# Optimization experiments

Measured on AMD Instinct MI355X. Metric: run time of the kernel, lower is better.

## Reference

```python
import jax, jax.numpy as jnp
import numpy as np

N = 65536          # total atoms
M = 12             # max neighbors
ORIG = 92          # orig_atom_fea_len
NBR = 41           # nbr_fea_len
AF = 64            # atom_fea_len
NCONV = 3
HF = 128           # h_fea_len
N0 = 1024          # number of crystals
EPS = 1e-5


def _glorot(key, shape):
    fan_in, fan_out = shape[0], shape[-1]
    lim = np.sqrt(6.0 / (fan_in + fan_out)).astype(np.float32)
    return jax.random.uniform(key, shape, jnp.float32, -lim, lim)


def setup_inputs() -> dict:
    key = jax.random.key(0)
    ks = jax.random.split(key, 16)
    atom_fea = jax.random.normal(ks[0], (N, ORIG), jnp.float32)
    nbr_fea = jax.random.normal(ks[1], (N, M, NBR), jnp.float32)
    nbr_fea_idx = jax.random.randint(ks[2], (N, M), 0, N, jnp.int32)
    # flat segment ids: ~64 atoms per crystal, contiguous (mimics ragged idx lists)
    crystal_idx = jnp.repeat(jnp.arange(N0, dtype=jnp.int32), N // N0)
    # parameters
    emb_w = _glorot(ks[3], (ORIG, AF)); emb_b = jnp.zeros((AF,), jnp.float32)
    conv_fc_w = _glorot(ks[4], (NCONV, 2 * AF + NBR, 2 * AF))
    conv_fc_b = jnp.zeros((NCONV, 2 * AF), jnp.float32)
    conv_bn1_g = jnp.ones((NCONV, 2 * AF), jnp.float32)
    conv_bn1_b = jnp.zeros((NCONV, 2 * AF), jnp.float32)
    conv_bn2_g = jnp.ones((NCONV, AF), jnp.float32)
    conv_bn2_b = jnp.zeros((NCONV, AF), jnp.float32)
    fc1_w = _glorot(ks[5], (AF, HF)); fc1_b = jnp.zeros((HF,), jnp.float32)
    out1_w = _glorot(ks[6], (HF, HF // 2)); out1_b = jnp.zeros((HF // 2,), jnp.float32)
    out2_w = _glorot(ks[7], (HF // 2, 1)); out2_b = jnp.zeros((1,), jnp.float32)
    return dict(atom_fea=atom_fea, nbr_fea=nbr_fea, nbr_fea_idx=nbr_fea_idx,
                crystal_idx=crystal_idx, emb_w=emb_w, emb_b=emb_b,
                conv_fc_w=conv_fc_w, conv_fc_b=conv_fc_b,
                conv_bn1_g=conv_bn1_g, conv_bn1_b=conv_bn1_b,
                conv_bn2_g=conv_bn2_g, conv_bn2_b=conv_bn2_b,
                fc1_w=fc1_w, fc1_b=fc1_b, out1_w=out1_w, out1_b=out1_b,
                out2_w=out2_w, out2_b=out2_b)


def _batchnorm(x, g, b):
    # training-mode BatchNorm1d over axis 0, biased variance, eps=1e-5
    mu = jnp.mean(x, axis=0)
    var = jnp.var(x, axis=0)
    return (x - mu) * jax.lax.rsqrt(var + EPS) * g + b


def _conv_layer(afea, nbr_fea, nbr_idx, w, b, g1, b1, g2, b2):
    # gather neighbor atom features: (N, M, AF)
    atom_nbr = afea[nbr_idx]
    self_fea = jnp.broadcast_to(afea[:, None, :], (N, M, AF))
    total = jnp.concatenate([self_fea, atom_nbr, nbr_fea], axis=-1)  # (N, M, 2AF+NBR)
    gated = jnp.einsum('nmf,fg->nmg', total, w) + b                  # (N, M, 2AF)
    gated = _batchnorm(gated.reshape(-1, 2 * AF), g1, b1).reshape(N, M, 2 * AF)
    filt, core = jnp.split(gated, 2, axis=-1)
    nbr_sumed = jnp.sum(jax.nn.sigmoid(filt) * jax.nn.softplus(core), axis=1)  # scatter-sum over nbrs
    nbr_sumed = _batchnorm(nbr_sumed, g2, b2)
    return jax.nn.softplus(afea + nbr_sumed)


def reference(atom_fea, nbr_fea, nbr_fea_idx, crystal_idx, emb_w, emb_b,
              conv_fc_w, conv_fc_b, conv_bn1_g, conv_bn1_b, conv_bn2_g, conv_bn2_b,
              fc1_w, fc1_b, out1_w, out1_b, out2_w, out2_b):
    afea = atom_fea @ emb_w + emb_b                 # (N, AF)
    identity = afea
    for i in range(NCONV):
        afea = _conv_layer(afea, nbr_fea, nbr_fea_idx,
                           conv_fc_w[i], conv_fc_b[i],
                           conv_bn1_g[i], conv_bn1_b[i],
                           conv_bn2_g[i], conv_bn2_b[i])
        afea = afea + identity
        identity = afea
    # ragged per-crystal mean pooling via segment_sum
    sums = jax.ops.segment_sum(afea, crystal_idx, num_segments=N0)
    counts = jax.ops.segment_sum(jnp.ones((N,), afea.dtype), crystal_idx, num_segments=N0)
    crys = sums / jnp.maximum(counts, 1.0)[:, None]  # (N0, AF)
    crys = jax.nn.softplus(crys) @ fc1_w + fc1_b
    crys = jax.nn.softplus(crys)                     # (N0, HF) == repr
    out = jax.nn.softplus(crys @ out1_w + out1_b) @ out2_w + out2_b  # (N0, 1)
    return out, crys
```

## Files before the change

### kernel.cpp

```cpp
#include <hip/hip_runtime.h>

#define NATOM 65536
#define MNBR 12
#define NMROW (NATOM*MNBR)
#define ORIG 92
#define NBRF 41
#define AF 64
#define HF 128
#define NCRYS 1024
#define EPSBN 1e-5f
#define NBP 48
#define CGRID 2048
#define NTASK 16384

typedef __attribute__((ext_vector_type(8))) short short8;
typedef __attribute__((ext_vector_type(4))) float floatx4;

__device__ __forceinline__ float softplusf_(float x){
    return fmaxf(x,0.f) + __logf(1.f + __expf(-fabsf(x)));
}
__device__ __forceinline__ float sigmoidf_(float x){
    return __builtin_amdgcn_rcpf(1.f + __expf(-x));
}
__device__ __forceinline__ short f2bf(float x){
    unsigned u = __float_as_uint(x);
    u += 0x7fffu + ((u >> 16) & 1u);
    return (short)(u >> 16);
}

__global__ void k_embed(const float* __restrict__ atom_fea, const float* __restrict__ emb_w,
                        const float* __restrict__ emb_b, float* __restrict__ afea,
                        short* __restrict__ abf)
{
    __shared__ float wl[ORIG*AF];
    __shared__ float bl[AF];
    __shared__ float rows[4*ORIG];
    int tid = threadIdx.x;
    for (int i = tid; i < ORIG*AF; i += 256) wl[i] = emb_w[i];
    if (tid < AF) bl[tid] = emb_b[tid];
    __syncthreads();
    for (int t = blockIdx.x; t < NATOM/4; t += gridDim.x) {
        for (int i = tid; i < 4*ORIG; i += 256) rows[i] = atom_fea[t*4*ORIG + i];
        __syncthreads();
        int r = tid >> 6, c = tid & 63;
        float acc = bl[c];
        const float* rp = &rows[r*ORIG];
        #pragma unroll 4
        for (int k = 0; k < ORIG; ++k) acc += rp[k] * wl[k*AF + c];
        int n = t*4 + r;
        afea[n*AF + c] = acc;
        abf[n*AF + c] = f2bf(acc);
        __syncthreads();
    }
}

__global__ void k_prep_nbr(const float* __restrict__ nbr_fea, short* __restrict__ nbf)
{
    int g = blockIdx.x*256 + threadIdx.x;
    int row = g / NBP, k = g % NBP;
    float v = (k < NBRF) ? nbr_fea[row*NBRF + k] : 0.f;
    nbf[g] = f2bf(v);
}

__global__ void k_prep_w(const float* __restrict__ W, short* __restrict__ wt2)
{
    int g = blockIdx.x*256 + threadIdx.x;
    int j = g & 7, c = (g >> 3) & 127, q = (g >> 10) & 3, ks = g >> 12;
    int k = ks*32 + q*8 + j;
    wt2[g] = (k < 169) ? f2bf(W[k*128 + c]) : (short)0;
}

template<int PASS2>
__global__ __launch_bounds__(256, 3)
void k_conv(const short* __restrict__ abf, const short* __restrict__ nbf,
            const int* __restrict__ nbr_idx, const short* __restrict__ wt2,
            const float* __restrict__ bias,
            float* __restrict__ stats1, const float* __restrict__ bn1ss,
            float* __restrict__ nsum, float* __restrict__ stats2)
{
    __shared__ __align__(16) short stg[2][6432];
    __shared__ float pbuf[4*12*17];

    int tid = threadIdx.x;
    int lane = tid & 63, wave = tid >> 6;
    int l15 = lane & 15, q = lane >> 4;
    int cf = wave*16 + l15;
    int cc = 64 + cf;

    short8 wf[6][2];
    #pragma unroll
    for (int ks = 0; ks < 6; ++ks) {
        wf[ks][0] = *(const short8*)(wt2 + ((ks*4+q)*128 + cf)*8);
        wf[ks][1] = *(const short8*)(wt2 + ((ks*4+q)*128 + cc)*8);
    }
    float bs0 = bias[cf], bs1 = bias[cc];
    float sc0=0.f, sh0=0.f, sc1=0.f, sh1=0.f;
    if (PASS2) { sc0=bn1ss[cf]; sh0=bn1ss[128+cf]; sc1=bn1ss[cc]; sh1=bn1ss[128+cc]; }

    int kind[3], ldso[3], nrow[3]; long gco[3];
    #pragma unroll
    for (int s = 0; s < 3; ++s) {
        int i = tid + s*256;
        if (i < 384)      { kind[s]=0; int row=i>>3, c=i&7; nrow[s]=row; ldso[s]=row*72+c*8; gco[s]=c*8; }
        else if (i < 672) { kind[s]=1; int j=i-384; int row=j/6, c=j%6; nrow[s]=0; ldso[s]=3456+row*56+c*8; gco[s]=row*48+c*8; }
        else if (i < 704) { kind[s]=2; int j=i-672; int a=j>>3, c=j&7; nrow[s]=0; ldso[s]=6144+a*72+c*8; gco[s]=a*64+c*8; }
        else              { kind[s]=3; nrow[s]=0; ldso[s]=0; gco[s]=0; }
    }
    int art[3], nvo[3], evo[3], svo[3];
    #pragma unroll
    for (int rt = 0; rt < 3; ++rt) {
        int r = rt*16 + l15;
        art[rt] = r/12;
        nvo[rt] = r*72 + q*8;
        evo[rt] = 3456 + r*56 + q*8;
        svo[rt] = 6144 + art[rt]*72 + q*8;
    }

    float s_acc[2]={0.f,0.f}, s2_acc[2]={0.f,0.f};
    float st2s = 0.f, st2q = 0.f;
    const short8 zf = {0,0,0,0,0,0,0,0};
    float* pb = pbuf + wave*(12*17);
    const int bt = blockIdx.x;

    int nid[3];
    short8 hold[3];
    #pragma unroll
    for (int s = 0; s < 3; ++s)
        if (kind[s]==0) nid[s] = nbr_idx[bt*48 + nrow[s]];
    #pragma unroll
    for (int s = 0; s < 3; ++s) {
        if (kind[s]==0)      hold[s] = *(const short8*)(abf + (unsigned)nid[s]*64u + gco[s]);
        else if (kind[s]==1) hold[s] = *(const short8*)(nbf + (long)bt*2304 + gco[s]);
        else if (kind[s]==2) hold[s] = *(const short8*)(abf + (unsigned)bt*256u + gco[s]);
    }
    #pragma unroll
    for (int s = 0; s < 3; ++s)
        if (kind[s]==0) nid[s] = nbr_idx[(bt+CGRID)*48 + nrow[s]];
    #pragma unroll
    for (int s = 0; s < 3; ++s)
        if (kind[s] < 3) *(short8*)(&stg[0][0] + ldso[s]) = hold[s];
    __syncthreads();

    #pragma unroll 2
    for (int k = 0; k < 8; ++k) {
        int b = bt + k*CGRID;
        if (k < 7) {
            int bn = b + CGRID;
            #pragma unroll
            for (int s = 0; s < 3; ++s) {
                if (kind[s]==0)      hold[s] = *(const short8*)(abf + (unsigned)nid[s]*64u + gco[s]);
                else if (kind[s]==1) hold[s] = *(const short8*)(nbf + (long)bn*2304 + gco[s]);
                else if (kind[s]==2) hold[s] = *(const short8*)(abf + (unsigned)bn*256u + gco[s]);
            }
            if (k < 6) {
                #pragma unroll
                for (int s = 0; s < 3; ++s)
                    if (kind[s]==0) nid[s] = nbr_idx[(bn+CGRID)*48 + nrow[s]];
            }
        }

        const short* sb = &stg[k & 1][0];
        floatx4 acc[3][2];
        #pragma unroll
        for (int rt=0; rt<3; ++rt) {
            acc[rt][0] = (floatx4){bs0,bs0,bs0,bs0};
            acc[rt][1] = (floatx4){bs1,bs1,bs1,bs1};
        }
        #pragma unroll
        for (int rt = 0; rt < 3; ++rt) {
            short8 sv0 = *(const short8*)(sb + svo[rt]);
            short8 sv1 = *(const short8*)(sb + svo[rt] + 32);
            short8 nv0 = *(const short8*)(sb + nvo[rt]);
            short8 nv1 = *(const short8*)(sb + nvo[rt] + 32);
            short8 ev0 = *(const short8*)(sb + evo[rt]);
            short8 ev1 = (q < 2) ? *(const short8*)(sb + evo[rt] + 32) : zf;
            #pragma unroll
            for (int ct = 0; ct < 2; ++ct) {
                acc[rt][ct] = __builtin_amdgcn_mfma_f32_16x16x32_bf16(sv0, wf[0][ct], acc[rt][ct], 0,0,0);
                acc[rt][ct] = __builtin_amdgcn_mfma_f32_16x16x32_bf16(sv1, wf[1][ct], acc[rt][ct], 0,0,0);
                acc[rt][ct] = __builtin_amdgcn_mfma_f32_16x16x32_bf16(nv0, wf[2][ct], acc[rt][ct], 0,0,0);
                acc[rt][ct] = __builtin_amdgcn_mfma_f32_16x16x32_bf16(nv1, wf[3][ct], acc[rt][ct], 0,0,0);
                acc[rt][ct] = __builtin_amdgcn_mfma_f32_16x16x32_bf16(ev0, wf[4][ct], acc[rt][ct], 0,0,0);
                acc[rt][ct] = __builtin_amdgcn_mfma_f32_16x16x32_bf16(ev1, wf[5][ct], acc[rt][ct], 0,0,0);
            }
        }

        if (!PASS2) {
            #pragma unroll
            for (int ct=0; ct<2; ++ct)
                #pragma unroll
                for (int rt=0; rt<3; ++rt)
                    #pragma unroll
                    for (int r=0; r<4; ++r) {
                        float v = acc[rt][ct][r];
                        s_acc[ct] += v; s2_acc[ct] += v*v;
                    }
        } else {
            #pragma unroll
            for (int rt=0; rt<3; ++rt) {
                float part = 0.f;
                #pragma unroll
                for (int r=0; r<4; ++r) {
                    float f = acc[rt][0][r]*sc0 + sh0;
                    float g = acc[rt][1][r]*sc1 + sh1;
                    part += sigmoidf_(f) * softplusf_(g);
                }
                pb[(rt*4+q)*17 + l15] = part;
            }
            int a = lane >> 4, c16 = lane & 15;
            float s = pb[(3*a+0)*17 + c16] + pb[(3*a+1)*17 + c16] + pb[(3*a+2)*17 + c16];
            nsum[(b*4 + a)*AF + wave*16 + c16] = s;
            st2s += s; st2q += s*s;
        }

        if (k < 7) {
            short* db = &stg[(k + 1) & 1][0];
            #pragma unroll
            for (int s = 0; s < 3; ++s)
                if (kind[s] < 3) *(short8*)(db + ldso[s]) = hold[s];
        }
        __syncthreads();
    }

    if (!PASS2) {
        #pragma unroll
        for (int ct=0; ct<2; ++ct) {
            float s = s_acc[ct], s2 = s2_acc[ct];
            s  += __shfl_xor(s, 16);  s  += __shfl_xor(s, 32);
            s2 += __shfl_xor(s2, 16); s2 += __shfl_xor(s2, 32);
            if (q == 0) {
                int c = ct ? cc : cf;
                atomicAdd(&stats1[c], s);
                atomicAdd(&stats1[128 + c], s2);
            }
        }
    } else {
        st2s += __shfl_xor(st2s, 16); st2s += __shfl_xor(st2s, 32);
        st2q += __shfl_xor(st2q, 16); st2q += __shfl_xor(st2q, 32);
        if (q == 0) {
            atomicAdd(&stats2[cf], st2s);
            atomicAdd(&stats2[64 + cf], st2q);
        }
    }
}

__global__ void k_bn1fin(const float* __restrict__ stats1, const float* __restrict__ g,
                         const float* __restrict__ b, float* __restrict__ bn1ss)
{
    int c = threadIdx.x;
    float mean = stats1[c] * (1.f/NMROW);
    float var  = stats1[128+c] * (1.f/NMROW) - mean*mean;
    float scale = g[c] * rsqrtf(var + EPSBN);
    bn1ss[c] = scale;
    bn1ss[128+c] = b[c] - mean*scale;
}

__global__ void k_update(float* __restrict__ afea, short* __restrict__ abf,
                         const float* __restrict__ nsum,
                         const float* __restrict__ stats2,
                         const float* __restrict__ g2, const float* __restrict__ b2)
{
    int g = blockIdx.x*256 + threadIdx.x;
    int c = g & 63;
    float mean = stats2[c] * (1.f/NATOM);
    float var  = stats2[64+c] * (1.f/NATOM) - mean*mean;
    float scale = g2[c]*rsqrtf(var + EPSBN);
    float shift = b2[c] - mean*scale;
    float ns = nsum[g]*scale + shift;
    float a = afea[g];
    float v = softplusf_(a + ns) + a;
    afea[g] = v; abf[g] = f2bf(v);
}

__global__ void k_pool(const float* __restrict__ afea, const int* __restrict__ cidx,
                       float* __restrict__ pool, float* __restrict__ cnt)
{
    int g = blockIdx.x*256 + threadIdx.x;
    int c = g & 63; int chunk = g >> 6;
    float run = 0.f, rc = 0.f; int cur = -1;
    for (int i = 0; i < 16; ++i) {
        int a = chunk*16 + i;
        int cr = cidx[a];
        float v = afea[a*64 + c];
        if (cr != cur) {
            if (cur >= 0) { atomicAdd(&pool[cur*64+c], run); if (c==0) atomicAdd(&cnt[cur], rc); }
            run = 0.f; rc = 0.f; cur = cr;
        }
        run += v; rc += 1.f;
    }
    atomicAdd(&pool[cur*64+c], run); if (c==0) atomicAdd(&cnt[cur], rc);
}

__global__ void k_head(const float* __restrict__ pool, const float* __restrict__ cnt,
                       const float* __restrict__ fc1w, const float* __restrict__ fc1b,
                       const float* __restrict__ o1w, const float* __restrict__ o1b,
                       const float* __restrict__ o2w, const float* __restrict__ o2b,
                       float* __restrict__ dout)
{
    __shared__ float spv[64], crys[128], h1[64];
    int b = blockIdx.x, tid = threadIdx.x;
    if (tid < 64) {
        float ct = fmaxf(cnt[b], 1.f);
        spv[tid] = softplusf_(pool[b*64+tid] / ct);
    }
    __syncthreads();
    float a = fc1b[tid];
    for (int k = 0; k < 64; ++k) a += spv[k] * fc1w[k*128 + tid];
    float v = softplusf_(a);
    crys[tid] = v;
    dout[NCRYS + b*128 + tid] = v;
    __syncthreads();
    if (tid < 64) {
        float a2 = o1b[tid];
        for (int k = 0; k < 128; ++k) a2 += crys[k] * o1w[k*64 + tid];
        h1[tid] = softplusf_(a2) * o2w[tid];
    }
    __syncthreads();
    if (tid == 0) {
        float s = o2b[0];
        for (int j = 0; j < 64; ++j) s += h1[j];
        dout[b] = s;
    }
}

extern "C" void kernel_launch(void* const* d_in, const int* in_sizes, int n_in,
                              void* d_out, int out_size, void* d_ws, size_t ws_size,
                              hipStream_t stream)
{
    const float* atom_fea = (const float*)d_in[0];
    const float* nbr_fea  = (const float*)d_in[1];
    const int*   nbr_idx  = (const int*)d_in[2];
    const int*   cidx     = (const int*)d_in[3];
    const float* emb_w    = (const float*)d_in[4];
    const float* emb_b    = (const float*)d_in[5];
    const float* cfw      = (const float*)d_in[6];
    const float* cfb      = (const float*)d_in[7];
    const float* bn1g     = (const float*)d_in[8];
    const float* bn1b     = (const float*)d_in[9];
    const float* bn2g     = (const float*)d_in[10];
    const float* bn2b     = (const float*)d_in[11];
    const float* fc1w     = (const float*)d_in[12];
    const float* fc1b     = (const float*)d_in[13];
    const float* o1w      = (const float*)d_in[14];
    const float* o1b      = (const float*)d_in[15];
    const float* o2w      = (const float*)d_in[16];
    const float* o2b      = (const float*)d_in[17];

    float* ws    = (float*)d_ws;
    float* afea  = ws;
    float* nsum  = ws + 4194304;
    short* abf   = (short*)(ws + 8388608);
    short* nbf   = (short*)(ws + 10485760);
    short* wt2   = (short*)(ws + 29360128);
    float* stats = ws + 29372416;
    float* pool  = ws + 29374336;
    float* cnt   = ws + 29439872;

    hipMemsetAsync(stats, 0, (1920 + 65536 + 1024)*sizeof(float), stream);

    k_prep_nbr<<<(NMROW*NBP)/256, 256, 0, stream>>>(nbr_fea, nbf);
    k_embed<<<2048, 256, 0, stream>>>(atom_fea, emb_w, emb_b, afea, abf);

    for (int L = 0; L < 3; ++L) {
        float* st1 = stats + L*640;
        float* ss  = st1 + 256;
        float* st2 = st1 + 512;
        k_prep_w<<<96, 256, 0, stream>>>(cfw + L*169*128, wt2);
        k_conv<0><<<CGRID, 256, 0, stream>>>(abf, nbf, nbr_idx, wt2, cfb + L*128, st1, nullptr, nullptr, nullptr);
        k_bn1fin<<<1, 128, 0, stream>>>(st1, bn1g + L*128, bn1b + L*128, ss);
        k_conv<1><<<CGRID, 256, 0, stream>>>(abf, nbf, nbr_idx, wt2, cfb + L*128, nullptr, ss, nsum, st2);
        k_update<<<16384, 256, 0, stream>>>(afea, abf, nsum, st2, bn2g + L*64, bn2b + L*64);
    }
    k_pool<<<1024, 256, 0, stream>>>(afea, cidx, pool, cnt);
    k_head<<<NCRYS, 128, 0, stream>>>(pool, cnt, fc1w, fc1b, o1w, o1b, o2w, o2b, (float*)d_out);
}
```

Before: 849.7 us.

## Store conv gate pre-activations in bf16 instead of recomputing the conv GEMM

The first conv pass now writes the filter and core pre-activations as packed bf16 pairs to a large workspace buffer. A new lightweight gate kernel then applies BN1, sigmoid and softplus and sums over neighbors, replacing the second full gather-plus-MFMA pass. This trades a recomputed GEMM and gather for about 200 MB of extra write and read traffic per layer, and it rounds the pre-activations to bf16 before BN. The neighbor-feature prep kernel is also vectorised to write 8 bf16 values per thread. The old two-pass path is kept as a fallback when the workspace is too small.

```diff
diff --git a/kernel.cpp b/kernel.cpp
--- a/kernel.cpp
+++ b/kernel.cpp
@@ -27,6 +27,9 @@
     u += 0x7fffu + ((u >> 16) & 1u);
     return (short)(u >> 16);
 }
+__device__ __forceinline__ unsigned packbf(float f, float g){
+    return (unsigned)(unsigned short)f2bf(f) | ((unsigned)(unsigned short)f2bf(g) << 16);
+}
 
 __global__ void k_embed(const float* __restrict__ atom_fea, const float* __restrict__ emb_w,
                         const float* __restrict__ emb_b, float* __restrict__ afea,
@@ -57,9 +60,16 @@
 __global__ void k_prep_nbr(const float* __restrict__ nbr_fea, short* __restrict__ nbf)
 {
     int g = blockIdx.x*256 + threadIdx.x;
-    int row = g / NBP, k = g % NBP;
-    float v = (k < NBRF) ? nbr_fea[row*NBRF + k] : 0.f;
-    nbf[g] = f2bf(v);
+    int row = g / 6, c = g % 6;
+    const float* src = nbr_fea + (long)row*NBRF + c*8;
+    short8 v = {0,0,0,0,0,0,0,0};
+    if (c < 5) {
+        #pragma unroll
+        for (int j = 0; j < 8; ++j) v[j] = f2bf(src[j]);
+    } else {
+        v[0] = f2bf(src[0]);
+    }
+    *(short8*)(nbf + (long)g*8) = v;
 }
 
 __global__ void k_prep_w(const float* __restrict__ W, short* __restrict__ wt2)
@@ -70,16 +80,17 @@
     wt2[g] = (k < 169) ? f2bf(W[k*128 + c]) : (short)0;
 }
 
-template<int PASS2>
+template<int MODE>
 __global__ __launch_bounds__(256, 3)
 void k_conv(const short* __restrict__ abf, const short* __restrict__ nbf,
             const int* __restrict__ nbr_idx, const short* __restrict__ wt2,
             const float* __restrict__ bias,
             float* __restrict__ stats1, const float* __restrict__ bn1ss,
-            float* __restrict__ nsum, float* __restrict__ stats2)
+            float* __restrict__ nsum, float* __restrict__ stats2,
+            unsigned* __restrict__ gpair)
 {
     __shared__ __align__(16) short stg[2][6432];
-    __shared__ float pbuf[4*12*17];
+    __shared__ float pbuf[(MODE==1) ? 4*12*17 : 4];
 
     int tid = threadIdx.x;
     int lane = tid & 63, wave = tid >> 6;
@@ -95,7 +106,7 @@
     }
     float bs0 = bias[cf], bs1 = bias[cc];
     float sc0=0.f, sh0=0.f, sc1=0.f, sh1=0.f;
-    if (PASS2) { sc0=bn1ss[cf]; sh0=bn1ss[128+cf]; sc1=bn1ss[cc]; sh1=bn1ss[128+cc]; }
+    if (MODE==1) { sc0=bn1ss[cf]; sh0=bn1ss[128+cf]; sc1=bn1ss[cc]; sh1=bn1ss[128+cc]; }
 
     int kind[3], ldso[3], nrow[3]; long gco[3];
     #pragma unroll
@@ -119,7 +130,7 @@
     float s_acc[2]={0.f,0.f}, s2_acc[2]={0.f,0.f};
     float st2s = 0.f, st2q = 0.f;
     const short8 zf = {0,0,0,0,0,0,0,0};
-    float* pb = pbuf + wave*(12*17);
+    float* pb = pbuf + ((MODE==1) ? wave*(12*17) : 0);
     const int bt = blockIdx.x;
 
     int nid[3];
@@ -185,7 +196,7 @@
             }
         }
 
-        if (!PASS2) {
+        if (MODE != 1) {
             #pragma unroll
             for (int ct=0; ct<2; ++ct)
                 #pragma unroll
@@ -195,7 +206,17 @@
                         float v = acc[rt][ct][r];
                         s_acc[ct] += v; s2_acc[ct] += v*v;
                     }
-        } else {
+        }
+        if (MODE == 2) {
+            #pragma unroll
+            for (int rt=0; rt<3; ++rt) {
+                unsigned base = (unsigned)(b*48 + rt*16 + q*4)*64u + (unsigned)(wave*16 + l15);
+                #pragma unroll
+                for (int r=0; r<4; ++r)
+                    gpair[base + (unsigned)r*64u] = packbf(acc[rt][0][r], acc[rt][1][r]);
+            }
+        }
+        if (MODE == 1) {
             #pragma unroll
             for (int rt=0; rt<3; ++rt) {
                 float part = 0.f;
@@ -222,7 +243,7 @@
         __syncthreads();
     }
 
-    if (!PASS2) {
+    if (MODE != 1) {
         #pragma unroll
         for (int ct=0; ct<2; ++ct) {
             float s = s_acc[ct], s2 = s2_acc[ct];
@@ -241,6 +262,46 @@
             atomicAdd(&stats2[cf], st2s);
             atomicAdd(&stats2[64 + cf], st2q);
         }
+    }
+}
+
+__global__ __launch_bounds__(256, 4)
+void k_gate(const unsigned* __restrict__ gpair, const float* __restrict__ bn1ss,
+            float* __restrict__ nsum, float* __restrict__ stats2)
+{
+    __shared__ float red[2][4][64];
+    int tid = threadIdx.x;
+    int lane = tid & 63, wave = tid >> 6;
+    float scf = bn1ss[lane],    shf = bn1ss[128+lane];
+    float scc = bn1ss[64+lane], shc = bn1ss[192+lane];
+    float st2s = 0.f, st2q = 0.f;
+    int a0 = blockIdx.x*64 + wave;
+    for (int j = 0; j < 16; ++j) {
+        int atom = a0 + j*4;
+        const unsigned* gp = gpair + (unsigned)atom*12u*64u + lane;
+        unsigned u[12];
+        #pragma unroll
+        for (int i = 0; i < 12; ++i) u[i] = gp[i*64];
+        float s = 0.f;
+        #pragma unroll
+        for (int i = 0; i < 12; ++i) {
+            float f = __uint_as_float(u[i] << 16);
+            float g = __uint_as_float(u[i] & 0xffff0000u);
+            f = f*scf + shf;
+            g = g*scc + shc;
+            s += sigmoidf_(f) * softplusf_(g);
+        }
+        nsum[atom*AF + lane] = s;
+        st2s += s; st2q += s*s;
+    }
+    red[0][wave][lane] = st2s;
+    red[1][wave][lane] = st2q;
+    __syncthreads();
+    if (tid < 64) {
+        float s  = red[0][0][tid] + red[0][1][tid] + red[0][2][tid] + red[0][3][tid];
+        float s2 = red[1][0][tid] + red[1][1][tid] + red[1][2][tid] + red[1][3][tid];
+        atomicAdd(&stats2[tid], s);
+        atomicAdd(&stats2[64 + tid], s2);
     }
 }
 
@@ -355,10 +416,13 @@
     float* stats = ws + 29372416;
     float* pool  = ws + 29374336;
     float* cnt   = ws + 29439872;
+    unsigned* gpair = (unsigned*)(ws + 29440896);
+
+    bool big = ws_size >= (size_t)(29440896 + 50331648) * 4;
 
     hipMemsetAsync(stats, 0, (1920 + 65536 + 1024)*sizeof(float), stream);
 
-    k_prep_nbr<<<(NMROW*NBP)/256, 256, 0, stream>>>(nbr_fea, nbf);
+    k_prep_nbr<<<(NMROW*6)/256, 256, 0, stream>>>(nbr_fea, nbf);
     k_embed<<<2048, 256, 0, stream>>>(atom_fea, emb_w, emb_b, afea, abf);
 
     for (int L = 0; L < 3; ++L) {
@@ -366,9 +430,18 @@
         float* ss  = st1 + 256;
         float* st2 = st1 + 512;
         k_prep_w<<<96, 256, 0, stream>>>(cfw + L*169*128, wt2);
-        k_conv<0><<<CGRID, 256, 0, stream>>>(abf, nbf, nbr_idx, wt2, cfb + L*128, st1, nullptr, nullptr, nullptr);
-        k_bn1fin<<<1, 128, 0, stream>>>(st1, bn1g + L*128, bn1b + L*128, ss);
-        k_conv<1><<<CGRID, 256, 0, stream>>>(abf, nbf, nbr_idx, wt2, cfb + L*128, nullptr, ss, nsum, st2);
+        if (big) {
+            k_conv<2><<<CGRID, 256, 0, stream>>>(abf, nbf, nbr_idx, wt2, cfb + L*128,
+                                                 st1, nullptr, nullptr, nullptr, gpair);
+            k_bn1fin<<<1, 128, 0, stream>>>(st1, bn1g + L*128, bn1b + L*128, ss);
+            k_gate<<<NATOM/64, 256, 0, stream>>>(gpair, ss, nsum, st2);
+        } else {
+            k_conv<0><<<CGRID, 256, 0, stream>>>(abf, nbf, nbr_idx, wt2, cfb + L*128,
+                                                 st1, nullptr, nullptr, nullptr, nullptr);
+            k_bn1fin<<<1, 128, 0, stream>>>(st1, bn1g + L*128, bn1b + L*128, ss);
+            k_conv<1><<<CGRID, 256, 0, stream>>>(abf, nbf, nbr_idx, wt2, cfb + L*128,
+                                                 nullptr, ss, nsum, st2, nullptr);
+        }
         k_update<<<16384, 256, 0, stream>>>(afea, abf, nsum, st2, bn2g + L*64, bn2b + L*64);
     }
     k_pool<<<1024, 256, 0, stream>>>(afea, cidx, pool, cnt);
```

Result: faster. 821.6 us (-3.3%).

## Split conv output channels across 8 waves and vectorize prep/update kernels

Applied to the files above, without the earlier changes.

The conv kernel moves from 256 to 512 threads per block. Each wave now computes one 16-channel column tile (filter or core half) instead of two, which halves its MFMA accumulator and weight registers. In pass 2 the filter waves write sigmoid values to shared memory and the core waves combine them after an extra barrier. The nbr prep and update kernels are vectorized to 8-wide and 4-wide stores, and the edge-feature loads become nontemporal. This aims to raise occupancy and latency hiding, at the cost of an extra __syncthreads and a shared-memory exchange per tile.

```diff
diff --git a/kernel.cpp b/kernel.cpp
--- a/kernel.cpp
+++ b/kernel.cpp
@@ -14,6 +14,7 @@
 #define NTASK 16384
 
 typedef __attribute__((ext_vector_type(8))) short short8;
+typedef __attribute__((ext_vector_type(4))) short shortx4;
 typedef __attribute__((ext_vector_type(4))) float floatx4;
 
 __device__ __forceinline__ float softplusf_(float x){
@@ -57,9 +58,16 @@
 __global__ void k_prep_nbr(const float* __restrict__ nbr_fea, short* __restrict__ nbf)
 {
     int g = blockIdx.x*256 + threadIdx.x;
-    int row = g / NBP, k = g % NBP;
-    float v = (k < NBRF) ? nbr_fea[row*NBRF + k] : 0.f;
-    nbf[g] = f2bf(v);
+    int row = g / 6, c = g % 6;
+    const float* src = nbr_fea + (long)row*NBRF + c*8;
+    short8 v = {0,0,0,0,0,0,0,0};
+    if (c < 5) {
+        #pragma unroll
+        for (int j = 0; j < 8; ++j) v[j] = f2bf(src[j]);
+    } else {
+        v[0] = f2bf(src[0]);
+    }
+    *(short8*)(nbf + (long)g*8) = v;
 }
 
 __global__ void k_prep_w(const float* __restrict__ W, short* __restrict__ wt2)
@@ -71,7 +79,7 @@
 }
 
 template<int PASS2>
-__global__ __launch_bounds__(256, 3)
+__global__ __launch_bounds__(512, 4)
 void k_conv(const short* __restrict__ abf, const short* __restrict__ nbf,
             const int* __restrict__ nbr_idx, const short* __restrict__ wt2,
             const float* __restrict__ bias,
@@ -79,65 +87,61 @@
             float* __restrict__ nsum, float* __restrict__ stats2)
 {
     __shared__ __align__(16) short stg[2][6432];
-    __shared__ float pbuf[4*12*17];
+    __shared__ float xbuf[PASS2 ? 48*68 : 4];
+    __shared__ float pbuf[PASS2 ? 4*12*17 : 4];
 
     int tid = threadIdx.x;
     int lane = tid & 63, wave = tid >> 6;
     int l15 = lane & 15, q = lane >> 4;
-    int cf = wave*16 + l15;
-    int cc = 64 + cf;
-
-    short8 wf[6][2];
-    #pragma unroll
-    for (int ks = 0; ks < 6; ++ks) {
-        wf[ks][0] = *(const short8*)(wt2 + ((ks*4+q)*128 + cf)*8);
-        wf[ks][1] = *(const short8*)(wt2 + ((ks*4+q)*128 + cc)*8);
-    }
-    float bs0 = bias[cf], bs1 = bias[cc];
-    float sc0=0.f, sh0=0.f, sc1=0.f, sh1=0.f;
-    if (PASS2) { sc0=bn1ss[cf]; sh0=bn1ss[128+cf]; sc1=bn1ss[cc]; sh1=bn1ss[128+cc]; }
-
-    int kind[3], ldso[3], nrow[3]; long gco[3];
-    #pragma unroll
-    for (int s = 0; s < 3; ++s) {
-        int i = tid + s*256;
+    int isCore = wave >> 2;
+    int wgrp = wave & 3;
+    int cp = wgrp*16 + l15;
+    int ch = isCore*64 + cp;
+
+    short8 wf[6];
+    #pragma unroll
+    for (int ks = 0; ks < 6; ++ks)
+        wf[ks] = *(const short8*)(wt2 + ((ks*4+q)*128 + ch)*8);
+    float bs = bias[ch];
+    float sc = 0.f, sh = 0.f;
+    if (PASS2) { sc = bn1ss[ch]; sh = bn1ss[128+ch]; }
+
+    int kind[2], ldso[2], nrow[2], gco[2];
+    #pragma unroll
+    for (int s = 0; s < 2; ++s) {
+        int i = tid + s*512;
         if (i < 384)      { kind[s]=0; int row=i>>3, c=i&7; nrow[s]=row; ldso[s]=row*72+c*8; gco[s]=c*8; }
         else if (i < 672) { kind[s]=1; int j=i-384; int row=j/6, c=j%6; nrow[s]=0; ldso[s]=3456+row*56+c*8; gco[s]=row*48+c*8; }
         else if (i < 704) { kind[s]=2; int j=i-672; int a=j>>3, c=j&7; nrow[s]=0; ldso[s]=6144+a*72+c*8; gco[s]=a*64+c*8; }
         else              { kind[s]=3; nrow[s]=0; ldso[s]=0; gco[s]=0; }
     }
-    int art[3], nvo[3], evo[3], svo[3];
+    int nvo[3], evo[3], svo[3];
     #pragma unroll
     for (int rt = 0; rt < 3; ++rt) {
         int r = rt*16 + l15;
-        art[rt] = r/12;
         nvo[rt] = r*72 + q*8;
         evo[rt] = 3456 + r*56 + q*8;
-        svo[rt] = 6144 + art[rt]*72 + q*8;
-    }
-
-    float s_acc[2]={0.f,0.f}, s2_acc[2]={0.f,0.f};
+        svo[rt] = 6144 + (r/12)*72 + q*8;
+    }
+
+    float s_acc = 0.f, s2_acc = 0.f;
     float st2s = 0.f, st2q = 0.f;
     const short8 zf = {0,0,0,0,0,0,0,0};
-    float* pb = pbuf + wave*(12*17);
+    float* pb = pbuf + (PASS2 ? wgrp*(12*17) : 0);
     const int bt = blockIdx.x;
 
-    int nid[3];
-    short8 hold[3];
-    #pragma unroll
-    for (int s = 0; s < 3; ++s)
-        if (kind[s]==0) nid[s] = nbr_idx[bt*48 + nrow[s]];
-    #pragma unroll
-    for (int s = 0; s < 3; ++s) {
-        if (kind[s]==0)      hold[s] = *(const short8*)(abf + (unsigned)nid[s]*64u + gco[s]);
-        else if (kind[s]==1) hold[s] = *(const short8*)(nbf + (long)bt*2304 + gco[s]);
+    int nid = 0;
+    short8 hold[2];
+    if (kind[0]==0) nid = nbr_idx[bt*48 + nrow[0]];
+    #pragma unroll
+    for (int s = 0; s < 2; ++s) {
+        if (kind[s]==0)      hold[s] = *(const short8*)(abf + (unsigned)nid*64u + gco[s]);
+        else if (kind[s]==1) hold[s] = __builtin_nontemporal_load((const short8*)(nbf + (long)bt*2304 + gco[s]));
         else if (kind[s]==2) hold[s] = *(const short8*)(abf + (unsigned)bt*256u + gco[s]);
     }
-    #pragma unroll
-    for (int s = 0; s < 3; ++s)
-        if (kind[s]==0) nid[s] = nbr_idx[(bt+CGRID)*48 + nrow[s]];
-    #pragma unroll
-    for (int s = 0; s < 3; ++s)
+    if (kind[0]==0) nid = nbr_idx[(bt+CGRID)*48 + nrow[0]];
+    #pragma unroll
+    for (int s = 0; s < 2; ++s)
         if (kind[s] < 3) *(short8*)(&stg[0][0] + ldso[s]) = hold[s];
     __syncthreads();
 
@@ -147,25 +151,18 @@
         if (k < 7) {
             int bn = b + CGRID;
             #pragma unroll
-            for (int s = 0; s < 3; ++s) {
-                if (kind[s]==0)      hold[s] = *(const short8*)(abf + (unsigned)nid[s]*64u + gco[s]);
-                else if (kind[s]==1) hold[s] = *(const short8*)(nbf + (long)bn*2304 + gco[s]);
+            for (int s = 0; s < 2; ++s) {
+                if (kind[s]==0)      hold[s] = *(const short8*)(abf + (unsigned)nid*64u + gco[s]);
+                else if (kind[s]==1) hold[s] = __builtin_nontemporal_load((const short8*)(nbf + (long)bn*2304 + gco[s]));
                 else if (kind[s]==2) hold[s] = *(const short8*)(abf + (unsigned)bn*256u + gco[s]);
             }
-            if (k < 6) {
-                #pragma unroll
-                for (int s = 0; s < 3; ++s)
-                    if (kind[s]==0) nid[s] = nbr_idx[(bn+CGRID)*48 + nrow[s]];
-            }
+            if (k < 6 && kind[0]==0) nid = nbr_idx[(bn+CGRID)*48 + nrow[0]];
         }
 
         const short* sb = &stg[k & 1][0];
-        floatx4 acc[3][2];
+        floatx4 acc[3];
         #pragma unroll
-        for (int rt=0; rt<3; ++rt) {
-            acc[rt][0] = (floatx4){bs0,bs0,bs0,bs0};
-            acc[rt][1] = (floatx4){bs1,bs1,bs1,bs1};
-        }
+        for (int rt=0; rt<3; ++rt) acc[rt] = (floatx4){bs,bs,bs,bs};
         #pragma unroll
         for (int rt = 0; rt < 3; ++rt) {
             short8 sv0 = *(const short8*)(sb + svo[rt]);
@@ -174,72 +171,74 @@
             short8 nv1 = *(const short8*)(sb + nvo[rt] + 32);
             short8 ev0 = *(const short8*)(sb + evo[rt]);
             short8 ev1 = (q < 2) ? *(const short8*)(sb + evo[rt] + 32) : zf;
-            #pragma unroll
-            for (int ct = 0; ct < 2; ++ct) {
-                acc[rt][ct] = __builtin_amdgcn_mfma_f32_16x16x32_bf16(sv0, wf[0][ct], acc[rt][ct], 0,0,0);
-                acc[rt][ct] = __builtin_amdgcn_mfma_f32_16x16x32_bf16(sv1, wf[1][ct], acc[rt][ct], 0,0,0);
-                acc[rt][ct] = __builtin_amdgcn_mfma_f32_16x16x32_bf16(nv0, wf[2][ct], acc[rt][ct], 0,0,0);
-                acc[rt][ct] = __builtin_amdgcn_mfma_f32_16x16x32_bf16(nv1, wf[3][ct], acc[rt][ct], 0,0,0);
-                acc[rt][ct] = __builtin_amdgcn_mfma_f32_16x16x32_bf16(ev0, wf[4][ct], acc[rt][ct], 0,0,0);
-                acc[rt][ct] = __builtin_amdgcn_mfma_f32_16x16x32_bf16(ev1, wf[5][ct], acc[rt][ct], 0,0,0);
-            }
+            acc[rt] = __builtin_amdgcn_mfma_f32_16x16x32_bf16(sv0, wf[0], acc[rt], 0,0,0);
+            acc[rt] = __builtin_amdgcn_mfma_f32_16x16x32_bf16(sv1, wf[1], acc[rt], 0,0,0);
+            acc[rt] = __builtin_amdgcn_mfma_f32_16x16x32_bf16(nv0, wf[2], acc[rt], 0,0,0);
+            acc[rt] = __builtin_amdgcn_mfma_f32_16x16x32_bf16(nv1, wf[3], acc[rt], 0,0,0);
+            acc[rt] = __builtin_amdgcn_mfma_f32_16x16x32_bf16(ev0, wf[4], acc[rt], 0,0,0);
+            acc[rt] = __builtin_amdgcn_mfma_f32_16x16x32_bf16(ev1, wf[5], acc[rt], 0,0,0);
         }
 
         if (!PASS2) {
             #pragma unroll
-            for (int ct=0; ct<2; ++ct)
+            for (int rt=0; rt<3; ++rt)
+                #pragma unroll
+                for (int r=0; r<4; ++r) {
+                    float v = acc[rt][r];
+                    s_acc += v; s2_acc += v*v;
+                }
+        } else {
+            if (!isCore) {
                 #pragma unroll
                 for (int rt=0; rt<3; ++rt)
                     #pragma unroll
                     for (int r=0; r<4; ++r) {
-                        float v = acc[rt][ct][r];
-                        s_acc[ct] += v; s2_acc[ct] += v*v;
+                        int row = rt*16 + q*4 + r;
+                        xbuf[row*68 + cp] = sigmoidf_(acc[rt][r]*sc + sh);
                     }
-        } else {
-            #pragma unroll
-            for (int rt=0; rt<3; ++rt) {
-                float part = 0.f;
+            }
+            __syncthreads();
+            if (isCore) {
                 #pragma unroll
-                for (int r=0; r<4; ++r) {
-                    float f = acc[rt][0][r]*sc0 + sh0;
-                    float g = acc[rt][1][r]*sc1 + sh1;
-                    part += sigmoidf_(f) * softplusf_(g);
+                for (int rt=0; rt<3; ++rt) {
+                    float part = 0.f;
+                    #pragma unroll
+                    for (int r=0; r<4; ++r) {
+                        int row = rt*16 + q*4 + r;
+                        part += xbuf[row*68 + cp] * softplusf_(acc[rt][r]*sc + sh);
+                    }
+                    pb[(rt*4+q)*17 + l15] = part;
                 }
-                pb[(rt*4+q)*17 + l15] = part;
+                int a = lane >> 4, c16 = lane & 15;
+                float s = pb[(3*a+0)*17 + c16] + pb[(3*a+1)*17 + c16] + pb[(3*a+2)*17 + c16];
+                nsum[(b*4 + a)*AF + wgrp*16 + c16] = s;
+                st2s += s; st2q += s*s;
             }
-            int a = lane >> 4, c16 = lane & 15;
-            float s = pb[(3*a+0)*17 + c16] + pb[(3*a+1)*17 + c16] + pb[(3*a+2)*17 + c16];
-            nsum[(b*4 + a)*AF + wave*16 + c16] = s;
-            st2s += s; st2q += s*s;
         }
 
         if (k < 7) {
             short* db = &stg[(k + 1) & 1][0];
             #pragma unroll
-            for (int s = 0; s < 3; ++s)
+            for (int s = 0; s < 2; ++s)
                 if (kind[s] < 3) *(short8*)(db + ldso[s]) = hold[s];
         }
         __syncthreads();
     }
 
     if (!PASS2) {
-        #pragma unroll
-        for (int ct=0; ct<2; ++ct) {
-            float s = s_acc[ct], s2 = s2_acc[ct];
-            s  += __shfl_xor(s, 16);  s  += __shfl_xor(s, 32);
-            s2 += __shfl_xor(s2, 16); s2 += __shfl_xor(s2, 32);
-            if (q == 0) {
-                int c = ct ? cc : cf;
-                atomicAdd(&stats1[c], s);
-                atomicAdd(&stats1[128 + c], s2);
-            }
-        }
-    } else {
+        float s = s_acc, s2 = s2_acc;
+        s  += __shfl_xor(s, 16);  s  += __shfl_xor(s, 32);
+        s2 += __shfl_xor(s2, 16); s2 += __shfl_xor(s2, 32);
+        if (q == 0) {
+            atomicAdd(&stats1[ch], s);
+            atomicAdd(&stats1[128 + ch], s2);
+        }
+    } else if (isCore) {
         st2s += __shfl_xor(st2s, 16); st2s += __shfl_xor(st2s, 32);
         st2q += __shfl_xor(st2q, 16); st2q += __shfl_xor(st2q, 32);
         if (q == 0) {
-            atomicAdd(&stats2[cf], st2s);
-            atomicAdd(&stats2[64 + cf], st2q);
+            atomicAdd(&stats2[cp], st2s);
+            atomicAdd(&stats2[64 + cp], st2q);
         }
     }
 }
@@ -261,15 +260,24 @@
                          const float* __restrict__ g2, const float* __restrict__ b2)
 {
     int g = blockIdx.x*256 + threadIdx.x;
-    int c = g & 63;
-    float mean = stats2[c] * (1.f/NATOM);
-    float var  = stats2[64+c] * (1.f/NATOM) - mean*mean;
-    float scale = g2[c]*rsqrtf(var + EPSBN);
-    float shift = b2[c] - mean*scale;
-    float ns = nsum[g]*scale + shift;
-    float a = afea[g];
-    float v = softplusf_(a + ns) + a;
-    afea[g] = v; abf[g] = f2bf(v);
+    int c0 = (g*4) & 63;
+    float4 ns4 = ((const float4*)nsum)[g];
+    float4 a4  = ((const float4*)afea)[g];
+    float o[4]; shortx4 ob;
+    #pragma unroll
+    for (int i = 0; i < 4; ++i) {
+        int c = c0 + i;
+        float mean = stats2[c] * (1.f/NATOM);
+        float var  = stats2[64+c] * (1.f/NATOM) - mean*mean;
+        float scale = g2[c]*rsqrtf(var + EPSBN);
+        float shift = b2[c] - mean*scale;
+        float ns = ((const float*)&ns4)[i]*scale + shift;
+        float a = ((const float*)&a4)[i];
+        float v = softplusf_(a + ns) + a;
+        o[i] = v; ob[i] = f2bf(v);
+    }
+    ((float4*)afea)[g] = (float4){o[0],o[1],o[2],o[3]};
+    *(shortx4*)(abf + (long)g*4) = ob;
 }
 
 __global__ void k_pool(const float* __restrict__ afea, const int* __restrict__ cidx,
@@ -358,7 +366,7 @@
 
     hipMemsetAsync(stats, 0, (1920 + 65536 + 1024)*sizeof(float), stream);
 
-    k_prep_nbr<<<(NMROW*NBP)/256, 256, 0, stream>>>(nbr_fea, nbf);
+    k_prep_nbr<<<(NMROW*6)/256, 256, 0, stream>>>(nbr_fea, nbf);
     k_embed<<<2048, 256, 0, stream>>>(atom_fea, emb_w, emb_b, afea, abf);
 
     for (int L = 0; L < 3; ++L) {
@@ -366,10 +374,12 @@
         float* ss  = st1 + 256;
         float* st2 = st1 + 512;
         k_prep_w<<<96, 256, 0, stream>>>(cfw + L*169*128, wt2);
-        k_conv<0><<<CGRID, 256, 0, stream>>>(abf, nbf, nbr_idx, wt2, cfb + L*128, st1, nullptr, nullptr, nullptr);
+        k_conv<0><<<CGRID, 512, 0, stream>>>(abf, nbf, nbr_idx, wt2, cfb + L*128,
+                                             st1, nullptr, nullptr, nullptr);
         k_bn1fin<<<1, 128, 0, stream>>>(st1, bn1g + L*128, bn1b + L*128, ss);
-        k_conv<1><<<CGRID, 256, 0, stream>>>(abf, nbf, nbr_idx, wt2, cfb + L*128, nullptr, ss, nsum, st2);
-        k_update<<<16384, 256, 0, stream>>>(afea, abf, nsum, st2, bn2g + L*64, bn2b + L*64);
+        k_conv<1><<<CGRID, 512, 0, stream>>>(abf, nbf, nbr_idx, wt2, cfb + L*128,
+                                             nullptr, ss, nsum, st2);
+        k_update<<<4096, 256, 0, stream>>>(afea, abf, nsum, st2, bn2g + L*64, bn2b + L*64);
     }
     k_pool<<<1024, 256, 0, stream>>>(afea, cidx, pool, cnt);
     k_head<<<NCRYS, 128, 0, stream>>>(pool, cnt, fc1w, fc1b, o1w, o1b, o2w, o2b, (float*)d_out);
```

Result: no change. 845.1 us (-0.5%).

## Stream edge features directly to LDS, shrink staging, vectorize prep and update kernels

Applied to the files above, without the earlier changes.

The conv kernel now copies the bf16 neighbor-edge tile from global memory straight into LDS with global_load_lds, so edge data no longer passes through registers. The staging layout is tightened (edge rows at stride 48, self rows at stride 64) and pbuf is shrunk in pass 1, which cuts LDS use and lets launch bounds rise from 3 to 4 blocks per SU. The nbr prep kernel writes 8 bf16 values per thread and k_update processes float4s with a quarter of the blocks. The denser edge-row layout risks more LDS bank conflicts, and the higher occupancy target may force register spills.

```diff
diff --git a/kernel.cpp b/kernel.cpp
--- a/kernel.cpp
+++ b/kernel.cpp
@@ -14,6 +14,7 @@
 #define NTASK 16384
 
 typedef __attribute__((ext_vector_type(8))) short short8;
+typedef __attribute__((ext_vector_type(4))) short shortx4;
 typedef __attribute__((ext_vector_type(4))) float floatx4;
 
 __device__ __forceinline__ float softplusf_(float x){
@@ -26,6 +27,10 @@
     unsigned u = __float_as_uint(x);
     u += 0x7fffu + ((u >> 16) & 1u);
     return (short)(u >> 16);
+}
+__device__ __forceinline__ void gl2lds16(const void* g, void* l){
+    __builtin_amdgcn_global_load_lds((const __attribute__((address_space(1))) unsigned int*)g,
+                                     (__attribute__((address_space(3))) unsigned int*)l, 16, 0, 0);
 }
 
 __global__ void k_embed(const float* __restrict__ atom_fea, const float* __restrict__ emb_w,
@@ -57,9 +62,16 @@
 __global__ void k_prep_nbr(const float* __restrict__ nbr_fea, short* __restrict__ nbf)
 {
     int g = blockIdx.x*256 + threadIdx.x;
-    int row = g / NBP, k = g % NBP;
-    float v = (k < NBRF) ? nbr_fea[row*NBRF + k] : 0.f;
-    nbf[g] = f2bf(v);
+    int row = g / 6, c = g % 6;
+    const float* src = nbr_fea + (long)row*NBRF + c*8;
+    short8 v = {0,0,0,0,0,0,0,0};
+    if (c < 5) {
+        #pragma unroll
+        for (int j = 0; j < 8; ++j) v[j] = f2bf(src[j]);
+    } else {
+        v[0] = f2bf(src[0]);
+    }
+    *(short8*)(nbf + (long)g*8) = v;
 }
 
 __global__ void k_prep_w(const float* __restrict__ W, short* __restrict__ wt2)
@@ -71,15 +83,15 @@
 }
 
 template<int PASS2>
-__global__ __launch_bounds__(256, 3)
+__global__ __launch_bounds__(256, 4)
 void k_conv(const short* __restrict__ abf, const short* __restrict__ nbf,
             const int* __restrict__ nbr_idx, const short* __restrict__ wt2,
             const float* __restrict__ bias,
             float* __restrict__ stats1, const float* __restrict__ bn1ss,
             float* __restrict__ nsum, float* __restrict__ stats2)
 {
-    __shared__ __align__(16) short stg[2][6432];
-    __shared__ float pbuf[4*12*17];
+    __shared__ __align__(16) short stg[2][6016];
+    __shared__ float pbuf[PASS2 ? 4*12*17 : 4];
 
     int tid = threadIdx.x;
     int lane = tid & 63, wave = tid >> 6;
@@ -97,65 +109,63 @@
     float sc0=0.f, sh0=0.f, sc1=0.f, sh1=0.f;
     if (PASS2) { sc0=bn1ss[cf]; sh0=bn1ss[128+cf]; sc1=bn1ss[cc]; sh1=bn1ss[128+cc]; }
 
-    int kind[3], ldso[3], nrow[3]; long gco[3];
-    #pragma unroll
-    for (int s = 0; s < 3; ++s) {
-        int i = tid + s*256;
-        if (i < 384)      { kind[s]=0; int row=i>>3, c=i&7; nrow[s]=row; ldso[s]=row*72+c*8; gco[s]=c*8; }
-        else if (i < 672) { kind[s]=1; int j=i-384; int row=j/6, c=j%6; nrow[s]=0; ldso[s]=3456+row*56+c*8; gco[s]=row*48+c*8; }
-        else if (i < 704) { kind[s]=2; int j=i-672; int a=j>>3, c=j&7; nrow[s]=0; ldso[s]=6144+a*72+c*8; gco[s]=a*64+c*8; }
-        else              { kind[s]=3; nrow[s]=0; ldso[s]=0; gco[s]=0; }
-    }
-    int art[3], nvo[3], evo[3], svo[3];
+    int ldso[2], gco[2], nrow0 = tid >> 3, nrow1 = 32 + (tid >> 3);
+    ldso[0] = nrow0*72 + (tid & 7)*8;
+    gco[0]  = (tid & 7)*8;
+    if (tid < 128)      { ldso[1] = nrow1*72 + (tid & 7)*8; gco[1] = (tid & 7)*8; }
+    else if (tid < 160) { int j = tid - 128; ldso[1] = 5760 + (j>>3)*64 + (j&7)*8; gco[1] = j*8; }
+    else                { ldso[1] = -1; gco[1] = 0; }
+
+    int nvo[3], evo[3], svo[3];
     #pragma unroll
     for (int rt = 0; rt < 3; ++rt) {
         int r = rt*16 + l15;
-        art[rt] = r/12;
         nvo[rt] = r*72 + q*8;
-        evo[rt] = 3456 + r*56 + q*8;
-        svo[rt] = 6144 + art[rt]*72 + q*8;
+        evo[rt] = 3456 + r*48 + q*8;
+        svo[rt] = 5760 + (r/12)*64 + q*8;
     }
 
     float s_acc[2]={0.f,0.f}, s2_acc[2]={0.f,0.f};
     float st2s = 0.f, st2q = 0.f;
     const short8 zf = {0,0,0,0,0,0,0,0};
-    float* pb = pbuf + wave*(12*17);
+    float* pb = pbuf + (PASS2 ? wave*(12*17) : 0);
     const int bt = blockIdx.x;
 
-    int nid[3];
-    short8 hold[3];
-    #pragma unroll
-    for (int s = 0; s < 3; ++s)
-        if (kind[s]==0) nid[s] = nbr_idx[bt*48 + nrow[s]];
-    #pragma unroll
-    for (int s = 0; s < 3; ++s) {
-        if (kind[s]==0)      hold[s] = *(const short8*)(abf + (unsigned)nid[s]*64u + gco[s]);
-        else if (kind[s]==1) hold[s] = *(const short8*)(nbf + (long)bt*2304 + gco[s]);
-        else if (kind[s]==2) hold[s] = *(const short8*)(abf + (unsigned)bt*256u + gco[s]);
-    }
-    #pragma unroll
-    for (int s = 0; s < 3; ++s)
-        if (kind[s]==0) nid[s] = nbr_idx[(bt+CGRID)*48 + nrow[s]];
-    #pragma unroll
-    for (int s = 0; s < 3; ++s)
-        if (kind[s] < 3) *(short8*)(&stg[0][0] + ldso[s]) = hold[s];
+    int nid0 = nbr_idx[bt*48 + nrow0];
+    int nid1 = (tid < 128) ? nbr_idx[bt*48 + nrow1] : 0;
+    {
+        const short* eb = nbf + (long)bt*2304;
+        gl2lds16(eb + wave*512 + lane*8, &stg[0][3456 + wave*512]);
+        if (wave == 0 && lane < 32)
+            gl2lds16(eb + 2048 + lane*8, &stg[0][3456 + 2048]);
+        short8 h0 = *(const short8*)(abf + (unsigned)nid0*64u + gco[0]);
+        short8 h1 = zf;
+        if (tid < 128)      h1 = *(const short8*)(abf + (unsigned)nid1*64u + gco[1]);
+        else if (tid < 160) h1 = *(const short8*)(abf + (unsigned)bt*256u + gco[1]);
+        *(short8*)(&stg[0][0] + ldso[0]) = h0;
+        if (ldso[1] >= 0) *(short8*)(&stg[0][0] + ldso[1]) = h1;
+    }
+    nid0 = nbr_idx[(bt+CGRID)*48 + nrow0];
+    if (tid < 128) nid1 = nbr_idx[(bt+CGRID)*48 + nrow1];
     __syncthreads();
 
     #pragma unroll 2
     for (int k = 0; k < 8; ++k) {
         int b = bt + k*CGRID;
+        short8 h0 = zf, h1 = zf;
         if (k < 7) {
             int bn = b + CGRID;
-            #pragma unroll
-            for (int s = 0; s < 3; ++s) {
-                if (kind[s]==0)      hold[s] = *(const short8*)(abf + (unsigned)nid[s]*64u + gco[s]);
-                else if (kind[s]==1) hold[s] = *(const short8*)(nbf + (long)bn*2304 + gco[s]);
-                else if (kind[s]==2) hold[s] = *(const short8*)(abf + (unsigned)bn*256u + gco[s]);
-            }
+            short* db = &stg[(k + 1) & 1][0];
+            const short* eb = nbf + (long)bn*2304;
+            gl2lds16(eb + wave*512 + lane*8, db + 3456 + wave*512);
+            if (wave == 0 && lane < 32)
+                gl2lds16(eb + 2048 + lane*8, db + 3456 + 2048);
+            h0 = *(const short8*)(abf + (unsigned)nid0*64u + gco[0]);
+            if (tid < 128)      h1 = *(const short8*)(abf + (unsigned)nid1*64u + gco[1]);
+            else if (tid < 160) h1 = *(const short8*)(abf + (unsigned)bn*256u + gco[1]);
             if (k < 6) {
-                #pragma unroll
-                for (int s = 0; s < 3; ++s)
-                    if (kind[s]==0) nid[s] = nbr_idx[(bn+CGRID)*48 + nrow[s]];
+                nid0 = nbr_idx[(bn+CGRID)*48 + nrow0];
+                if (tid < 128) nid1 = nbr_idx[(bn+CGRID)*48 + nrow1];
             }
         }
 
@@ -215,9 +225,8 @@
 
         if (k < 7) {
             short* db = &stg[(k + 1) & 1][0];
-            #pragma unroll
-            for (int s = 0; s < 3; ++s)
-                if (kind[s] < 3) *(short8*)(db + ldso[s]) = hold[s];
+            *(short8*)(db + ldso[0]) = h0;
+            if (ldso[1] >= 0) *(short8*)(db + ldso[1]) = h1;
         }
         __syncthreads();
     }
@@ -261,15 +270,24 @@
                          const float* __restrict__ g2, const float* __restrict__ b2)
 {
     int g = blockIdx.x*256 + threadIdx.x;
-    int c = g & 63;
-    float mean = stats2[c] * (1.f/NATOM);
-    float var  = stats2[64+c] * (1.f/NATOM) - mean*mean;
-    float scale = g2[c]*rsqrtf(var + EPSBN);
-    float shift = b2[c] - mean*scale;
-    float ns = nsum[g]*scale + shift;
-    float a = afea[g];
-    float v = softplusf_(a + ns) + a;
-    afea[g] = v; abf[g] = f2bf(v);
+    int c0 = (g*4) & 63;
+    float4 ns4 = ((const float4*)nsum)[g];
+    float4 a4  = ((const float4*)afea)[g];
+    float o[4]; shortx4 ob;
+    #pragma unroll
+    for (int i = 0; i < 4; ++i) {
+        int c = c0 + i;
+        float mean = stats2[c] * (1.f/NATOM);
+        float var  = stats2[64+c] * (1.f/NATOM) - mean*mean;
+        float scale = g2[c]*rsqrtf(var + EPSBN);
+        float shift = b2[c] - mean*scale;
+        float ns = ((const float*)&ns4)[i]*scale + shift;
+        float a = ((const float*)&a4)[i];
+        float v = softplusf_(a + ns) + a;
+        o[i] = v; ob[i] = f2bf(v);
+    }
+    ((float4*)afea)[g] = (float4){o[0],o[1],o[2],o[3]};
+    *(shortx4*)(abf + (long)g*4) = ob;
 }
 
 __global__ void k_pool(const float* __restrict__ afea, const int* __restrict__ cidx,
@@ -358,7 +376,7 @@
 
     hipMemsetAsync(stats, 0, (1920 + 65536 + 1024)*sizeof(float), stream);
 
-    k_prep_nbr<<<(NMROW*NBP)/256, 256, 0, stream>>>(nbr_fea, nbf);
+    k_prep_nbr<<<(NMROW*6)/256, 256, 0, stream>>>(nbr_fea, nbf);
     k_embed<<<2048, 256, 0, stream>>>(atom_fea, emb_w, emb_b, afea, abf);
 
     for (int L = 0; L < 3; ++L) {
@@ -366,10 +384,12 @@
         float* ss  = st1 + 256;
         float* st2 = st1 + 512;
         k_prep_w<<<96, 256, 0, stream>>>(cfw + L*169*128, wt2);
-        k_conv<0><<<CGRID, 256, 0, stream>>>(abf, nbf, nbr_idx, wt2, cfb + L*128, st1, nullptr, nullptr, nullptr);
+        k_conv<0><<<CGRID, 256, 0, stream>>>(abf, nbf, nbr_idx, wt2, cfb + L*128,
+                                             st1, nullptr, nullptr, nullptr);
         k_bn1fin<<<1, 128, 0, stream>>>(st1, bn1g + L*128, bn1b + L*128, ss);
-        k_conv<1><<<CGRID, 256, 0, stream>>>(abf, nbf, nbr_idx, wt2, cfb + L*128, nullptr, ss, nsum, st2);
-        k_update<<<16384, 256, 0, stream>>>(afea, abf, nsum, st2, bn2g + L*64, bn2b + L*64);
+        k_conv<1><<<CGRID, 256, 0, stream>>>(abf, nbf, nbr_idx, wt2, cfb + L*128,
+                                             nullptr, ss, nsum, st2);
+        k_update<<<4096, 256, 0, stream>>>(afea, abf, nsum, st2, bn2g + L*64, bn2b + L*64);
     }
     k_pool<<<1024, 256, 0, stream>>>(afea, cidx, pool, cnt);
     k_head<<<NCRYS, 128, 0, stream>>>(pool, cnt, fc1w, fc1b, o1w, o1b, o2w, o2b, (float*)d_out);
```

Result: slower. 1.186 ms (+39.6%).
